# Optimization experiments

Measured on AMD Instinct MI355X. Metric: run time of the kernel, lower is better.

Reference implementation:

```python
import jax, jax.numpy as jnp
import numpy as np

# Sizes (must match setup_inputs)
N = 1024      # total residues (2 structures x 512)
B = 2         # num_structid
RPS = 512     # residues per sample
P = 32        # n_protein_patches
E_AB = B * P * P
E_ab = 131072 # downsampled residue-residue edges
DIM = 256
PDIM = 128
NB = 15       # distance RBF basis count
EPS = 1e-6


def _fourier(x, f):
    # GaussianFourierEncoding1D: x [..., 1], f [m] -> [..., 2m]
    ang = 2.0 * jnp.pi * x * f
    return jnp.concatenate([jnp.sin(ang), jnp.cos(ang)], axis=-1)


def _gelu_mlp(x, w1, b1, w2, b2):
    return jnp.dot(jax.nn.gelu(jnp.dot(x, w1) + b1), w2) + b2


def _frames(coords):
    # get_frame_matrix from N, CA, C atoms via Gram-Schmidt; coords [N,3,3]
    a, b, c = coords[:, 0], coords[:, 1], coords[:, 2]
    v1 = c - b
    v2 = a - b
    e1 = v1 / (jnp.linalg.norm(v1, axis=-1, keepdims=True) + EPS)
    u2 = v2 - e1 * jnp.sum(e1 * v2, axis=-1, keepdims=True)
    e2 = u2 / (jnp.linalg.norm(u2, axis=-1, keepdims=True) + EPS)
    e3 = jnp.cross(e1, e2)
    R = jnp.stack([e1, e2, e3], axis=-1)  # columns are the frame axes
    return R, b


def setup_inputs() -> dict:
    key = jax.random.key(0)
    ks = jax.random.split(key, 16)

    def lin(k, i, o):
        return (jax.random.normal(k, (i, o), jnp.float32) / np.sqrt(i)).astype(jnp.float32)

    # per-sample index offsets so gathers stay within each structure
    off_ab = (jnp.arange(E_ab) // (E_ab // B)).astype(jnp.int32) * RPS
    gather_idx_ab_a = jax.random.randint(ks[0], (E_ab,), 0, RPS, jnp.int32) + off_ab
    gather_idx_ab_b = jax.random.randint(ks[1], (E_ab,), 0, RPS, jnp.int32) + off_ab
    off_pid = (jnp.arange(B * P) // P).astype(jnp.int32) * RPS
    gather_idx_pid_a = jax.random.randint(ks[2], (B * P,), 0, RPS, jnp.int32) + off_pid

    return {
        "res_embedding_in": jax.random.normal(ks[3], (N, DIM), jnp.float32),
        "timestep_encoding_prot": jax.random.uniform(ks[4], (N, 1), jnp.float32),
        "input_protein_coords": jax.random.normal(ks[5], (N, 3, 3), jnp.float32) * 3.0,
        "time_freq": jax.random.normal(ks[6], (16,), jnp.float32),
        "chain_freq": jax.random.normal(ks[7], (PDIM // 4,), jnp.float32),
        "w1_res": lin(ks[8], DIM + 32, DIM),
        "b1_res": jnp.zeros((DIM,), jnp.float32),
        "w2_res": lin(ks[9], DIM, DIM),
        "b2_res": jnp.zeros((DIM,), jnp.float32),
        "w_geom": lin(ks[10], NB + 9 + 3, PDIM),
        "w1_edge": lin(ks[11], PDIM + PDIM // 2 + 2 * DIM, DIM),
        "b1_edge": jnp.zeros((DIM,), jnp.float32),
        "w2_edge": lin(ks[12], DIM, PDIM),
        "b2_edge": jnp.zeros((PDIM,), jnp.float32),
        "residue_index": (jnp.arange(N, dtype=jnp.int32) % 256),
        "res_chain_id": (jnp.arange(N, dtype=jnp.int32) // 256),
        "gather_idx_ab_a": gather_idx_ab_a,
        "gather_idx_ab_b": gather_idx_ab_b,
        "gather_idx_pid_a": gather_idx_pid_a,
    }


def reference(res_embedding_in, timestep_encoding_prot, input_protein_coords,
              time_freq, chain_freq,
              w1_res, b1_res, w2_res, b2_res,
              w_geom,
              w1_edge, b1_edge, w2_edge, b2_edge,
              residue_index, res_chain_id,
              gather_idx_ab_a, gather_idx_ab_b, gather_idx_pid_a):
    # residue representation: res_in_mlp(cat(emb, time_enc)) + emb
    te = _fourier(timestep_encoding_prot, time_freq)  # [N, 32]
    rep = _gelu_mlp(jnp.concatenate([res_embedding_in, te], axis=-1),
                    w1_res, b1_res, w2_res, b2_res) + res_embedding_in

    # patch-grid (AB) edge expansion, then merged edge list (ab first, AB second)
    pid = gather_idx_pid_a.reshape(B, P)
    AB_a = jnp.broadcast_to(pid[:, :, None], (B, P, P)).reshape(-1)
    AB_b = jnp.broadcast_to(pid[:, None, :], (B, P, P)).reshape(-1)
    src = jnp.concatenate([gather_idx_ab_a, AB_a])
    dst = jnp.concatenate([gather_idx_ab_b, AB_b])

    # chain relative positional encoding (_compute_chain_pe)
    ri = residue_index.astype(jnp.float32)
    disp = (ri[src] - ri[dst]) / 8.0                        # [E]
    rope = _fourier(disp[:, None], chain_freq) / (jnp.abs(disp) + 1.0)[:, None]
    rope = rope * (res_chain_id[src] == res_chain_id[dst])[:, None]  # [E, PDIM//2]

    # relative geometry encoding from backbone frames
    R, t = _frames(input_protein_coords)
    d = t[dst] - t[src]                                     # [E, 3]
    dist = jnp.sqrt(jnp.sum(d * d, axis=-1) + EPS)
    local = jnp.einsum('eik,ei->ek', R[src], d) / (dist + 1.0)[:, None]
    relrot = jnp.einsum('eia,eib->eab', R[src], R[dst]).reshape(-1, 9)
    centers = jnp.linspace(0.0, 20.0, NB)
    sig = 20.0 / NB
    rbf = jnp.exp(-0.5 * ((dist[:, None] - centers) / sig) ** 2)
    geom = jnp.dot(jnp.concatenate([rbf, relrot, local], axis=-1), w_geom)  # [E, PDIM]

    # pp_edge_embed(cat(geom, chain_pe, rep[src], rep[dst]))
    edge_in = jnp.concatenate([geom, rope, rep[src], rep[dst]], axis=-1)
    edge_reps = _gelu_mlp(edge_in, w1_edge, b1_edge, w2_edge, b2_edge)  # [E, PDIM]
    return edge_reps
```

## Files before the change

kernel.cpp:

```cpp
#include <hip/hip_runtime.h>


typedef __attribute__((ext_vector_type(8))) short short8;
typedef __attribute__((ext_vector_type(4))) float f32x4;

#define TWO_PI 6.283185307179586f
#define E_AB_TOT 131072

#define WS_RT    0
#define WS_REPB  49152
#define WS_W1F   573440
#define WS_W2F   884736
#define WS_PS    950272
#define WS_PD    1998848
#define WS_WG1   3047424

__device__ __forceinline__ unsigned short f2bf(float x){
  unsigned int u = __float_as_uint(x);
  u += 0x7fffu + ((u >> 16) & 1u);
  return (unsigned short)(u >> 16);
}

__device__ __forceinline__ unsigned int pack_bf16(float lo, float hi){
  unsigned int ul = __float_as_uint(lo), uh = __float_as_uint(hi);
  ul += 0x7fffu + ((ul >> 16) & 1u);
  uh += 0x7fffu + ((uh >> 16) & 1u);
  return __builtin_amdgcn_perm(uh, ul, 0x07060302);
}

__device__ __forceinline__ float gelu_s(float x){
  float s = x * x;
  float w = x * __builtin_fmaf(-0.1029437f, s, -2.30220847f);
  float e = __builtin_exp2f(w);
  return x * __builtin_amdgcn_rcpf(1.0f + e);
}

__global__ __launch_bounds__(256) void prep_k(
    const float* __restrict__ emb, const float* __restrict__ ts,
    const float* __restrict__ tf,  const float* __restrict__ w1,
    const float* __restrict__ b1,  const float* __restrict__ w2,
    const float* __restrict__ b2,  unsigned short* __restrict__ repb,
    const float* __restrict__ coords, float* __restrict__ RT,
    const float* __restrict__ wg, const float* __restrict__ w1e,
    unsigned short* __restrict__ w1f,
    const float* __restrict__ w2e, unsigned short* __restrict__ w2f,
    float* __restrict__ wg1){
  __shared__ float xt[288 * 12];
  __shared__ float ht[256 * 12];
  int blk = blockIdx.x, tid = threadIdx.x;
  if (blk < 128){
    int n0 = blk * 8;
    #pragma unroll
    for (int nd = 0; nd < 8; ++nd)
      xt[tid * 12 + nd] = emb[(n0 + nd) * 256 + tid];
    {
      int nd = tid >> 5, j = tid & 31;
      float ang = TWO_PI * ts[n0 + nd] * tf[j & 15];
      float s, c; __sincosf(ang, &s, &c);
      xt[(256 + j) * 12 + nd] = (j < 16) ? s : c;
    }
    __syncthreads();
    float acc[8];
    float bias1 = b1[tid];
    #pragma unroll
    for (int nd = 0; nd < 8; ++nd) acc[nd] = bias1;
    #pragma unroll 4
    for (int k = 0; k < 288; ++k){
      float w = w1[k * 256 + tid];
      f32x4 xa = *(const f32x4*)&xt[k * 12];
      f32x4 xb = *(const f32x4*)&xt[k * 12 + 4];
      acc[0] += xa[0]*w; acc[1] += xa[1]*w; acc[2] += xa[2]*w; acc[3] += xa[3]*w;
      acc[4] += xb[0]*w; acc[5] += xb[1]*w; acc[6] += xb[2]*w; acc[7] += xb[3]*w;
    }
    #pragma unroll
    for (int nd = 0; nd < 8; ++nd) ht[tid * 12 + nd] = gelu_s(acc[nd]);
    __syncthreads();
    float acc2[8];
    float bias2 = b2[tid];
    #pragma unroll
    for (int nd = 0; nd < 8; ++nd) acc2[nd] = bias2;
    #pragma unroll 4
    for (int k = 0; k < 256; ++k){
      float w = w2[k * 256 + tid];
      f32x4 ha = *(const f32x4*)&ht[k * 12];
      f32x4 hb = *(const f32x4*)&ht[k * 12 + 4];
      acc2[0] += ha[0]*w; acc2[1] += ha[1]*w; acc2[2] += ha[2]*w; acc2[3] += ha[3]*w;
      acc2[4] += hb[0]*w; acc2[5] += hb[1]*w; acc2[6] += hb[2]*w; acc2[7] += hb[3]*w;
    }
    #pragma unroll
    for (int nd = 0; nd < 8; ++nd)
      repb[(n0 + nd) * 256 + tid] = f2bf(acc2[nd] + xt[tid * 12 + nd]);
  } else if (blk < 132){
    int n = (blk - 128) * 256 + tid;
    const float* p = coords + n * 9;
    float ax=p[0],ay=p[1],az=p[2], bx=p[3],by=p[4],bz=p[5], cx=p[6],cy=p[7],cz=p[8];
    float v1x=cx-bx, v1y=cy-by, v1z=cz-bz;
    float v2x=ax-bx, v2y=ay-by, v2z=az-bz;
    float n1 = sqrtf(v1x*v1x+v1y*v1y+v1z*v1z) + 1e-6f;
    float e1x=v1x/n1, e1y=v1y/n1, e1z=v1z/n1;
    float dp = e1x*v2x + e1y*v2y + e1z*v2z;
    float u2x=v2x-e1x*dp, u2y=v2y-e1y*dp, u2z=v2z-e1z*dp;
    float n2 = sqrtf(u2x*u2x+u2y*u2y+u2z*u2z) + 1e-6f;
    float e2x=u2x/n2, e2y=u2y/n2, e2z=u2z/n2;
    float* r = RT + n * 12;
    r[0]=e1x; r[1]=e2x; r[2]=e1y*e2z - e1z*e2y;
    r[3]=e1y; r[4]=e2y; r[5]=e1z*e2x - e1x*e2z;
    r[6]=e1z; r[7]=e2z; r[8]=e1x*e2y - e1y*e2x;
    r[9]=bx;  r[10]=by; r[11]=bz;
  } else if (blk < 148){
    int u = (blk - 132) * 4 + (tid >> 6);
    int lane = tid & 63;
    int s = u >> 3, c = u & 7;
    int n  = c * 16 + (lane & 15);
    int kb = s * 32 + (lane >> 4) * 8;
    unsigned short* o = w2f + (((s * 8 + c) * 64) + lane) * 8;
    unsigned short vals[8];
    #pragma unroll
    for (int j = 0; j < 8; ++j)
      vals[j] = f2bf(w2e[(kb + j) * 128 + n]);
    *(uint4*)o = *(const uint4*)vals;
  } else if (blk < 220){
    int u = 16 + (blk - 148) * 4 + (tid >> 6);
    int lane = tid & 63;
    int s = u >> 4, c = u & 15;
    int n  = c * 16 + (lane & 15);
    int kb = s * 32 + (lane >> 4) * 8;
    unsigned short* o = w1f + (((s * 16 + c) * 64) + lane) * 8;
    unsigned short vals[8];
    for (int j = 0; j < 8; ++j){
      int k = kb + j;
      float val;
      if (k < 91)       val = w1e[(128 + k - 27)  * 256 + n];
      else if (k < 96)  val = 0.f;
      else if (k < 352) val = w1e[(192 + k - 96)  * 256 + n];
      else              val = w1e[(448 + k - 352) * 256 + n];
      vals[j] = f2bf(val);
    }
    *(uint4*)o = *(const uint4*)vals;
  } else {
    int b2_ = blk - 220;
    int n0 = b2_ * 16;
    float* slab = xt;
    #pragma unroll
    for (int i = 0; i < 8; ++i){
      int idx = tid + 256 * i;
      slab[idx] = w1e[(idx >> 4) * 256 + n0 + (idx & 15)];
    }
    __syncthreads();
    #pragma unroll
    for (int i = 0; i < 2; ++i){
      int o = tid + 256 * i;
      if (o < 432){
        int k = o >> 4, c = o & 15;
        float acc = 0.f;
        for (int j2 = 0; j2 < 128; ++j2)
          acc += wg[k * 128 + j2] * slab[j2 * 16 + c];
        wg1[k * 256 + n0 + c] = acc;
      }
    }
  }
}

__global__ __launch_bounds__(512) void proj_k(
    const unsigned short* __restrict__ repb,
    unsigned short* __restrict__ w1f,
    const float* __restrict__ b1e, const float* __restrict__ wg1,
    const float* __restrict__ w1e,
    float* __restrict__ ps, float* __restrict__ pd)
{
  if (blockIdx.x >= 32){
    int u = (blockIdx.x - 32) * 8 + (threadIdx.x >> 6);
    int lane = threadIdx.x & 63;
    int n  = u * 16 + (lane & 15);
    int kb = (lane >> 4) * 8;
    unsigned short* o = w1f + ((u * 64) + lane) * 8;
    unsigned short vals[8];
    #pragma unroll
    for (int j = 0; j < 8; ++j){
      int k = kb + j;
      float val = (k < 27) ? wg1[k * 256 + n] : w1e[(128 + k - 27) * 256 + n];
      vals[j] = f2bf(val);
    }
    *(uint4*)o = *(const uint4*)vals;
    return;
  }
  int part = blockIdx.x & 1;
  int nt   = blockIdx.x >> 1;
  int tid  = threadIdx.x, w = tid >> 6, lane = tid & 63;
  int c0 = w * 2, lr = lane & 15, quad = lane >> 4;
  int n0g = nt * 64;
  const short8* w1f8 = (const short8*)w1f;
  f32x4 acc[8];
  #pragma unroll
  for (int i = 0; i < 8; ++i) acc[i] = (f32x4){0.f, 0.f, 0.f, 0.f};
  int sb = 3 + part * 8;
  #pragma unroll
  for (int s = 0; s < 8; ++s){
    short8 a0 = w1f8[((sb + s) * 16 + c0 + 0) * 64 + lane];
    short8 a1 = w1f8[((sb + s) * 16 + c0 + 1) * 64 + lane];
    #pragma unroll
    for (int t = 0; t < 4; ++t){
      short8 b = *(const short8*)(repb + (n0g + t * 16 + lr) * 256 + s * 32 + quad * 8);
      acc[t]     = __builtin_amdgcn_mfma_f32_16x16x32_bf16(a0, b, acc[t],     0, 0, 0);
      acc[4 + t] = __builtin_amdgcn_mfma_f32_16x16x32_bf16(a1, b, acc[4 + t], 0, 0, 0);
    }
  }
  float* out = part ? pd : ps;
  #pragma unroll
  for (int c = 0; c < 2; ++c){
    f32x4 add = (f32x4){0.f, 0.f, 0.f, 0.f};
    if (!part) add = *(const f32x4*)(b1e + (c0 + c) * 16 + quad * 4);
    #pragma unroll
    for (int t = 0; t < 4; ++t){
      f32x4 v = acc[c * 4 + t];
      v[0] += add[0]; v[1] += add[1]; v[2] += add[2]; v[3] += add[3];
      *(f32x4*)(out + (n0g + t * 16 + lr) * 256 + w * 32 + quad * 8 + c * 4) = v;
    }
  }
}

__global__ __launch_bounds__(512, 8) void edge_k(
    const float* __restrict__ RT,  const float* __restrict__ cf,
    const int* __restrict__ resi, const int* __restrict__ chain,
    const int* __restrict__ gia,  const int* __restrict__ gib,
    const int* __restrict__ pid,
    const unsigned short* __restrict__ w1f, const unsigned short* __restrict__ w2f,
    const float* __restrict__ ps, const float* __restrict__ pd,
    const float* __restrict__ bias2,
    float* __restrict__ outp)
{
  __shared__ __align__(16) char smem[32768];
  __shared__ __align__(16) float rtbuf[128][12];
  __shared__ float scD[64];
  __shared__ float scI[64];
  __shared__ int lsrc[64];
  __shared__ int ldst[64];

  int tid = threadIdx.x;
  int e0  = blockIdx.x * 64;

  if (tid < 64){
    int e = e0 + tid, s_, d_;
    if (e < E_AB_TOT){ s_ = gia[e]; d_ = gib[e]; }
    else {
      int i = e - E_AB_TOT;
      int b = i >> 10, w_ = i & 1023;
      s_ = pid[b * 32 + (w_ >> 5)];
      d_ = pid[b * 32 + (w_ & 31)];
    }
    lsrc[tid] = s_; ldst[tid] = d_;
    float disp = ((float)resi[s_] - (float)resi[d_]) * 0.125f;
    scD[tid] = disp;
    scI[tid] = (chain[s_] == chain[d_]) ? 1.f / (fabsf(disp) + 1.f) : 0.f;
  } else if (tid < 192){
    int r  = tid - 64;
    int e  = e0 + (r & 63);
    int node;
    if (e < E_AB_TOT){ node = (r < 64) ? gia[e] : gib[e]; }
    else {
      int i = e - E_AB_TOT;
      int b = i >> 10, w_ = i & 1023;
      node = (r < 64) ? pid[b * 32 + (w_ >> 5)] : pid[b * 32 + (w_ & 31)];
    }
    const f32x4* p = (const f32x4*)(RT + node * 12);
    f32x4* q = (f32x4*)(&rtbuf[r][0]);
    q[0] = p[0]; q[1] = p[1]; q[2] = p[2];
  }
  __syncthreads();

  {
    #pragma unroll
    for (int it = 0; it < 4; ++it){
      int v = it * 512 + tid, ed = v >> 5, j = v & 31;
      float ang = TWO_PI * scD[ed] * cf[j];
      float s, c; __sincosf(ang, &s, &c);
      float inv = scI[ed];
      unsigned short* row = (unsigned short*)(smem + ed * 208);
      row[27 + j] = f2bf(s * inv);
      row[59 + j] = f2bf(c * inv);
    }
    #pragma unroll
    for (int it = 0; it < 2; ++it){
      int v = it * 512 + tid, ed = v >> 4, c = v & 15;
      float tx = rtbuf[64 + ed][9]  - rtbuf[ed][9];
      float ty = rtbuf[64 + ed][10] - rtbuf[ed][10];
      float tz = rtbuf[64 + ed][11] - rtbuf[ed][11];
      float dist = sqrtf(tx*tx + ty*ty + tz*tz + 1e-6f);
      if (c < 15){
        float z = (dist - (float)c * (20.f / 14.f)) * (15.f / 20.f);
        ((unsigned short*)(smem + ed * 208))[c] = f2bf(__expf(-0.5f * z * z));
      }
    }
    #pragma unroll
    for (int it = 0; it < 2; ++it){
      int v = it * 512 + tid, ed = v >> 4, cc = v & 15;
      if (cc < 12){
        const float* Rs = &rtbuf[ed][0];
        const float* Rd = &rtbuf[64 + ed][0];
        float val;
        if (cc < 9){
          int a  = (cc >= 6) ? 2 : ((cc >= 3) ? 1 : 0);
          int b_ = cc - 3 * a;
          val = Rs[a]*Rd[b_] + Rs[3+a]*Rd[3+b_] + Rs[6+a]*Rd[6+b_];
        } else {
          int k = cc - 9;
          float tx = Rd[9]-Rs[9], ty = Rd[10]-Rs[10], tz = Rd[11]-Rs[11];
          float dist = sqrtf(tx*tx + ty*ty + tz*tz + 1e-6f);
          val = (Rs[k]*tx + Rs[3+k]*ty + Rs[6+k]*tz) / (dist + 1.f);
        }
        ((unsigned short*)(smem + ed * 208))[15 + cc] = f2bf(val);
      }
    }
    {
      int ed = tid >> 3, c8 = tid & 7;
      ((unsigned short*)(smem + ed * 208))[91 + c8] = 0;
    }
  }
  __syncthreads();

  int w    = tid >> 6, lane = tid & 63;
  int c0   = w * 2;
  int lr   = lane & 15;
  int quad = lane >> 4, qoff = quad * 16;
  f32x4 acc[8];
  #pragma unroll
  for (int i = 0; i < 8; ++i) acc[i] = (f32x4){0.f, 0.f, 0.f, 0.f};
  const short8* w1f8 = (const short8*)w1f;

  #pragma unroll
  for (int s = 0; s < 3; ++s){
    short8 a0 = w1f8[(s * 16 + c0 + 0) * 64 + lane];
    short8 a1 = w1f8[(s * 16 + c0 + 1) * 64 + lane];
    short8 be0 = *(const short8*)(smem + ( 0 + lr) * 208 + s * 64 + qoff);
    short8 be1 = *(const short8*)(smem + (16 + lr) * 208 + s * 64 + qoff);
    short8 be2 = *(const short8*)(smem + (32 + lr) * 208 + s * 64 + qoff);
    short8 be3 = *(const short8*)(smem + (48 + lr) * 208 + s * 64 + qoff);
    acc[0] = __builtin_amdgcn_mfma_f32_16x16x32_bf16(a0, be0, acc[0], 0, 0, 0);
    acc[1] = __builtin_amdgcn_mfma_f32_16x16x32_bf16(a0, be1, acc[1], 0, 0, 0);
    acc[2] = __builtin_amdgcn_mfma_f32_16x16x32_bf16(a0, be2, acc[2], 0, 0, 0);
    acc[3] = __builtin_amdgcn_mfma_f32_16x16x32_bf16(a0, be3, acc[3], 0, 0, 0);
    acc[4] = __builtin_amdgcn_mfma_f32_16x16x32_bf16(a1, be0, acc[4], 0, 0, 0);
    acc[5] = __builtin_amdgcn_mfma_f32_16x16x32_bf16(a1, be1, acc[5], 0, 0, 0);
    acc[6] = __builtin_amdgcn_mfma_f32_16x16x32_bf16(a1, be2, acc[6], 0, 0, 0);
    acc[7] = __builtin_amdgcn_mfma_f32_16x16x32_bf16(a1, be3, acc[7], 0, 0, 0);
  }

  int offS[4], offD[4];
  #pragma unroll
  for (int t = 0; t < 4; ++t){
    offS[t] = lsrc[t * 16 + lr] * 256 + w * 32 + quad * 8;
    offD[t] = ldst[t * 16 + lr] * 256 + w * 32 + quad * 8;
  }
  __syncthreads();

  {
    char* Hb = smem;
    #pragma unroll
    for (int c = 0; c < 2; ++c){
      f32x4 pv[4], qv[4];
      #pragma unroll
      for (int t = 0; t < 4; ++t){
        pv[t] = *(const f32x4*)(ps + offS[t] + c * 4);
        qv[t] = *(const f32x4*)(pd + offD[t] + c * 4);
      }
      int n = (c0 + c) * 16 + quad * 4;
      #pragma unroll
      for (int t = 0; t < 4; ++t){
        int e = t * 16 + lr;
        f32x4 s4 = acc[c * 4 + t];
        float v0 = gelu_s(s4[0] + pv[t][0] + qv[t][0]);
        float v1 = gelu_s(s4[1] + pv[t][1] + qv[t][1]);
        float v2 = gelu_s(s4[2] + pv[t][2] + qv[t][2]);
        float v3 = gelu_s(s4[3] + pv[t][3] + qv[t][3]);
        uint2 p; p.x = pack_bf16(v0, v1); p.y = pack_bf16(v2, v3);
        *(uint2*)(Hb + ((e * 512 + n * 2) ^ ((e & 7) << 4))) = p;
      }
    }
  }
  __syncthreads();

  int c2 = (w & 3) * 2;
  int eb = (w >> 2) * 32;
  int hx = (lr & 7) << 4;
  f32x4 acc2[4];
  #pragma unroll
  for (int i = 0; i < 4; ++i) acc2[i] = (f32x4){0.f, 0.f, 0.f, 0.f};
  const short8* w2f8 = (const short8*)w2f;
  #pragma unroll
  for (int s = 0; s < 8; ++s){
    short8 aa0 = w2f8[(s * 8 + c2 + 0) * 64 + lane];
    short8 aa1 = w2f8[(s * 8 + c2 + 1) * 64 + lane];
    short8 h0 = *(const short8*)(smem + (((eb +  0 + lr) * 512 + s * 64 + qoff) ^ hx));
    short8 h1 = *(const short8*)(smem + (((eb + 16 + lr) * 512 + s * 64 + qoff) ^ hx));
    acc2[0] = __builtin_amdgcn_mfma_f32_16x16x32_bf16(aa0, h0, acc2[0], 0, 0, 0);
    acc2[1] = __builtin_amdgcn_mfma_f32_16x16x32_bf16(aa0, h1, acc2[1], 0, 0, 0);
    acc2[2] = __builtin_amdgcn_mfma_f32_16x16x32_bf16(aa1, h0, acc2[2], 0, 0, 0);
    acc2[3] = __builtin_amdgcn_mfma_f32_16x16x32_bf16(aa1, h1, acc2[3], 0, 0, 0);
  }

  {
    int n0 = c2 * 16 + quad * 4;
    f32x4 bz0 = *(const f32x4*)(bias2 + n0);
    f32x4 bz1 = *(const f32x4*)(bias2 + n0 + 16);
    float* og = outp + (size_t)e0 * 128;
    #pragma unroll
    for (int t = 0; t < 2; ++t){
      int e = eb + t * 16 + lr;
      f32x4 v0, v1;
      v0[0] = acc2[t][0] + bz0[0]; v0[1] = acc2[t][1] + bz0[1];
      v0[2] = acc2[t][2] + bz0[2]; v0[3] = acc2[t][3] + bz0[3];
      v1[0] = acc2[2 + t][0] + bz1[0]; v1[1] = acc2[2 + t][1] + bz1[1];
      v1[2] = acc2[2 + t][2] + bz1[2]; v1[3] = acc2[2 + t][3] + bz1[3];
      *(f32x4*)(og + (size_t)e * 128 + n0)      = v0;
      *(f32x4*)(og + (size_t)e * 128 + n0 + 16) = v1;
    }
  }
}

extern "C" void kernel_launch(void* const* d_in, const int* in_sizes, int n_in,
                              void* d_out, int out_size, void* d_ws, size_t ws_size,
                              hipStream_t stream) {
  const float* emb    = (const float*)d_in[0];
  const float* ts     = (const float*)d_in[1];
  const float* coords = (const float*)d_in[2];
  const float* tf     = (const float*)d_in[3];
  const float* cf     = (const float*)d_in[4];
  const float* w1r    = (const float*)d_in[5];
  const float* b1r    = (const float*)d_in[6];
  const float* w2r    = (const float*)d_in[7];
  const float* b2r    = (const float*)d_in[8];
  const float* wg     = (const float*)d_in[9];
  const float* w1e    = (const float*)d_in[10];
  const float* b1e    = (const float*)d_in[11];
  const float* w2e    = (const float*)d_in[12];
  const float* b2e    = (const float*)d_in[13];
  const int* resi     = (const int*)d_in[14];
  const int* chain    = (const int*)d_in[15];
  const int* gia      = (const int*)d_in[16];
  const int* gib      = (const int*)d_in[17];
  const int* pid      = (const int*)d_in[18];

  char* ws = (char*)d_ws;
  float* RT            = (float*)(ws + WS_RT);
  unsigned short* REPB = (unsigned short*)(ws + WS_REPB);
  unsigned short* W1F  = (unsigned short*)(ws + WS_W1F);
  unsigned short* W2F  = (unsigned short*)(ws + WS_W2F);
  float* PS            = (float*)(ws + WS_PS);
  float* PD            = (float*)(ws + WS_PD);
  float* WG1           = (float*)(ws + WS_WG1);
  float* outp          = (float*)d_out;

  hipLaunchKernelGGL(prep_k, dim3(236), dim3(256), 0, stream,
                     emb, ts, tf, w1r, b1r, w2r, b2r, REPB,
                     coords, RT, wg, w1e, W1F, w2e, W2F, WG1);
  hipLaunchKernelGGL(proj_k, dim3(34), dim3(512), 0, stream,
                     REPB, W1F, b1e, WG1, w1e, PS, PD);
  hipLaunchKernelGGL(edge_k, dim3(2080), dim3(512), 0, stream,
                     RT, cf, resi, chain, gia, gib, pid, W1F, W2F, PS, PD,
                     b2e, outp);
}
```

Before: 222.6 us.

## Prefetch projected gathers before MFMA, fuse geom-weight packing into prep, nontemporal output stores

The edge kernel now issues its gathered ps/pd loads before the first MFMA loop, so their latency overlaps with matrix work rather than sitting after it. The geometry-weight fold and its bf16 packing move from proj_k into prep_k through shared memory, which removes the WG1 workspace round trip and two proj_k blocks. The occupancy hint on edge_k drops from 8 to 4 to leave room for the 32 extra prefetch registers per thread, and output stores become nontemporal. The risk is lower occupancy reducing latency hiding elsewhere in the kernel.

```diff
diff --git a/kernel.cpp b/kernel.cpp
--- a/kernel.cpp
+++ b/kernel.cpp
@@ -13,7 +13,6 @@
 #define WS_W2F   884736
 #define WS_PS    950272
 #define WS_PD    1998848
-#define WS_WG1   3047424
 
 __device__ __forceinline__ unsigned short f2bf(float x){
   unsigned int u = __float_as_uint(x);
@@ -43,8 +42,7 @@
     const float* __restrict__ coords, float* __restrict__ RT,
     const float* __restrict__ wg, const float* __restrict__ w1e,
     unsigned short* __restrict__ w1f,
-    const float* __restrict__ w2e, unsigned short* __restrict__ w2f,
-    float* __restrict__ wg1){
+    const float* __restrict__ w2e, unsigned short* __restrict__ w2f){
   __shared__ float xt[288 * 12];
   __shared__ float ht[256 * 12];
   int blk = blockIdx.x, tid = threadIdx.x;
@@ -138,9 +136,10 @@
     }
     *(uint4*)o = *(const uint4*)vals;
   } else {
-    int b2_ = blk - 220;
-    int n0 = b2_ * 16;
+    int c = blk - 220;
+    int n0 = c * 16;
     float* slab = xt;
+    float* res  = ht;
     #pragma unroll
     for (int i = 0; i < 8; ++i){
       int idx = tid + 256 * i;
@@ -151,39 +150,37 @@
     for (int i = 0; i < 2; ++i){
       int o = tid + 256 * i;
       if (o < 432){
-        int k = o >> 4, c = o & 15;
+        int k = o >> 4, cc = o & 15;
         float acc = 0.f;
         for (int j2 = 0; j2 < 128; ++j2)
-          acc += wg[k * 128 + j2] * slab[j2 * 16 + c];
-        wg1[k * 256 + n0 + c] = acc;
+          acc += wg[k * 128 + j2] * slab[j2 * 16 + cc];
+        res[o] = acc;
       }
+    }
+    __syncthreads();
+    if (tid < 64){
+      int lane = tid;
+      int nn = lane & 15;
+      int kb = (lane >> 4) * 8;
+      unsigned short vals[8];
+      #pragma unroll
+      for (int j = 0; j < 8; ++j){
+        int k = kb + j;
+        float val = (k < 27) ? res[k * 16 + nn]
+                             : w1e[(128 + k - 27) * 256 + n0 + nn];
+        vals[j] = f2bf(val);
+      }
+      *(uint4*)(w1f + ((c * 64) + lane) * 8) = *(const uint4*)vals;
     }
   }
 }
 
 __global__ __launch_bounds__(512) void proj_k(
     const unsigned short* __restrict__ repb,
-    unsigned short* __restrict__ w1f,
-    const float* __restrict__ b1e, const float* __restrict__ wg1,
-    const float* __restrict__ w1e,
+    const unsigned short* __restrict__ w1f,
+    const float* __restrict__ b1e,
     float* __restrict__ ps, float* __restrict__ pd)
 {
-  if (blockIdx.x >= 32){
-    int u = (blockIdx.x - 32) * 8 + (threadIdx.x >> 6);
-    int lane = threadIdx.x & 63;
-    int n  = u * 16 + (lane & 15);
-    int kb = (lane >> 4) * 8;
-    unsigned short* o = w1f + ((u * 64) + lane) * 8;
-    unsigned short vals[8];
-    #pragma unroll
-    for (int j = 0; j < 8; ++j){
-      int k = kb + j;
-      float val = (k < 27) ? wg1[k * 256 + n] : w1e[(128 + k - 27) * 256 + n];
-      vals[j] = f2bf(val);
-    }
-    *(uint4*)o = *(const uint4*)vals;
-    return;
-  }
   int part = blockIdx.x & 1;
   int nt   = blockIdx.x >> 1;
   int tid  = threadIdx.x, w = tid >> 6, lane = tid & 63;
@@ -219,7 +216,7 @@
   }
 }
 
-__global__ __launch_bounds__(512, 8) void edge_k(
+__global__ __launch_bounds__(512, 4) void edge_k(
     const float* __restrict__ RT,  const float* __restrict__ cf,
     const int* __restrict__ resi, const int* __restrict__ chain,
     const int* __restrict__ gia,  const int* __restrict__ gib,
@@ -267,6 +264,11 @@
     q[0] = p[0]; q[1] = p[1]; q[2] = p[2];
   }
   __syncthreads();
+
+  int w    = tid >> 6, lane = tid & 63;
+  int c0   = w * 2;
+  int lr   = lane & 15;
+  int quad = lane >> 4, qoff = quad * 16;
 
   {
     #pragma unroll
@@ -316,12 +318,21 @@
       ((unsigned short*)(smem + ed * 208))[91 + c8] = 0;
     }
   }
+
+  f32x4 pv0[4], pv1[4], qv0[4], qv1[4];
+  {
+    #pragma unroll
+    for (int t = 0; t < 4; ++t){
+      int oS = lsrc[t * 16 + lr] * 256 + w * 32 + quad * 8;
+      int oD = ldst[t * 16 + lr] * 256 + w * 32 + quad * 8;
+      pv0[t] = *(const f32x4*)(ps + oS);
+      pv1[t] = *(const f32x4*)(ps + oS + 4);
+      qv0[t] = *(const f32x4*)(pd + oD);
+      qv1[t] = *(const f32x4*)(pd + oD + 4);
+    }
+  }
   __syncthreads();
 
-  int w    = tid >> 6, lane = tid & 63;
-  int c0   = w * 2;
-  int lr   = lane & 15;
-  int quad = lane >> 4, qoff = quad * 16;
   f32x4 acc[8];
   #pragma unroll
   for (int i = 0; i < 8; ++i) acc[i] = (f32x4){0.f, 0.f, 0.f, 0.f};
@@ -344,37 +355,29 @@
     acc[6] = __builtin_amdgcn_mfma_f32_16x16x32_bf16(a1, be2, acc[6], 0, 0, 0);
     acc[7] = __builtin_amdgcn_mfma_f32_16x16x32_bf16(a1, be3, acc[7], 0, 0, 0);
   }
-
-  int offS[4], offD[4];
-  #pragma unroll
-  for (int t = 0; t < 4; ++t){
-    offS[t] = lsrc[t * 16 + lr] * 256 + w * 32 + quad * 8;
-    offD[t] = ldst[t * 16 + lr] * 256 + w * 32 + quad * 8;
-  }
   __syncthreads();
 
   {
     char* Hb = smem;
     #pragma unroll
-    for (int c = 0; c < 2; ++c){
-      f32x4 pv[4], qv[4];
-      #pragma unroll
-      for (int t = 0; t < 4; ++t){
-        pv[t] = *(const f32x4*)(ps + offS[t] + c * 4);
-        qv[t] = *(const f32x4*)(pd + offD[t] + c * 4);
-      }
-      int n = (c0 + c) * 16 + quad * 4;
-      #pragma unroll
-      for (int t = 0; t < 4; ++t){
-        int e = t * 16 + lr;
-        f32x4 s4 = acc[c * 4 + t];
-        float v0 = gelu_s(s4[0] + pv[t][0] + qv[t][0]);
-        float v1 = gelu_s(s4[1] + pv[t][1] + qv[t][1]);
-        float v2 = gelu_s(s4[2] + pv[t][2] + qv[t][2]);
-        float v3 = gelu_s(s4[3] + pv[t][3] + qv[t][3]);
-        uint2 p; p.x = pack_bf16(v0, v1); p.y = pack_bf16(v2, v3);
-        *(uint2*)(Hb + ((e * 512 + n * 2) ^ ((e & 7) << 4))) = p;
-      }
+    for (int t = 0; t < 4; ++t){
+      int e = t * 16 + lr;
+      int n0 = c0 * 16 + quad * 4;
+      f32x4 s0 = acc[t];
+      float a0 = gelu_s(s0[0] + pv0[t][0] + qv0[t][0]);
+      float a1 = gelu_s(s0[1] + pv0[t][1] + qv0[t][1]);
+      float a2 = gelu_s(s0[2] + pv0[t][2] + qv0[t][2]);
+      float a3 = gelu_s(s0[3] + pv0[t][3] + qv0[t][3]);
+      uint2 p0; p0.x = pack_bf16(a0, a1); p0.y = pack_bf16(a2, a3);
+      *(uint2*)(Hb + ((e * 512 + n0 * 2) ^ ((e & 7) << 4))) = p0;
+      int n1 = (c0 + 1) * 16 + quad * 4;
+      f32x4 s1 = acc[4 + t];
+      float b0 = gelu_s(s1[0] + pv1[t][0] + qv1[t][0]);
+      float b1 = gelu_s(s1[1] + pv1[t][1] + qv1[t][1]);
+      float b2 = gelu_s(s1[2] + pv1[t][2] + qv1[t][2]);
+      float b3 = gelu_s(s1[3] + pv1[t][3] + qv1[t][3]);
+      uint2 p1; p1.x = pack_bf16(b0, b1); p1.y = pack_bf16(b2, b3);
+      *(uint2*)(Hb + ((e * 512 + n1 * 2) ^ ((e & 7) << 4))) = p1;
     }
   }
   __syncthreads();
@@ -411,8 +414,8 @@
       v0[2] = acc2[t][2] + bz0[2]; v0[3] = acc2[t][3] + bz0[3];
       v1[0] = acc2[2 + t][0] + bz1[0]; v1[1] = acc2[2 + t][1] + bz1[1];
       v1[2] = acc2[2 + t][2] + bz1[2]; v1[3] = acc2[2 + t][3] + bz1[3];
-      *(f32x4*)(og + (size_t)e * 128 + n0)      = v0;
-      *(f32x4*)(og + (size_t)e * 128 + n0 + 16) = v1;
+      __builtin_nontemporal_store(v0, (f32x4*)(og + (size_t)e * 128 + n0));
+      __builtin_nontemporal_store(v1, (f32x4*)(og + (size_t)e * 128 + n0 + 16));
     }
   }
 }
@@ -447,14 +450,13 @@
   unsigned short* W2F  = (unsigned short*)(ws + WS_W2F);
   float* PS            = (float*)(ws + WS_PS);
   float* PD            = (float*)(ws + WS_PD);
-  float* WG1           = (float*)(ws + WS_WG1);
   float* outp          = (float*)d_out;
 
   hipLaunchKernelGGL(prep_k, dim3(236), dim3(256), 0, stream,
                      emb, ts, tf, w1r, b1r, w2r, b2r, REPB,
-                     coords, RT, wg, w1e, W1F, w2e, W2F, WG1);
-  hipLaunchKernelGGL(proj_k, dim3(34), dim3(512), 0, stream,
-                     REPB, W1F, b1e, WG1, w1e, PS, PD);
+                     coords, RT, wg, w1e, W1F, w2e, W2F);
+  hipLaunchKernelGGL(proj_k, dim3(32), dim3(512), 0, stream,
+                     REPB, W1F, b1e, PS, PD);
   hipLaunchKernelGGL(edge_k, dim3(2080), dim3(512), 0, stream,
                      RT, cf, resi, chain, gia, gib, pid, W1F, W2F, PS, PD,
                      b2e, outp);
```

Result: slower. 233.5 us (+4.9%).

## Fuse geometry-weight packing into prep, halve residue MLP rows per block

Applied to the files above, without the earlier changes.

The residue MLP in prep_k now handles 4 residues per block across 256 blocks instead of 8 across 128, giving more parallelism to the small dense stage. The fused geometry weight (w_geom times w1_edge slice) is now packed straight into the bf16 MFMA fragment layout inside prep_k, which removes the WG1 workspace round trip and the extra blocks in proj_k. The edge kernel's shared buffer grows and its launch-bounds occupancy hint drops from 8 to 4, which changes register allocation and may reduce resident waves.

```diff
diff --git a/kernel.cpp b/kernel.cpp
--- a/kernel.cpp
+++ b/kernel.cpp
@@ -13,7 +13,6 @@
 #define WS_W2F   884736
 #define WS_PS    950272
 #define WS_PD    1998848
-#define WS_WG1   3047424
 
 __device__ __forceinline__ unsigned short f2bf(float x){
   unsigned int u = __float_as_uint(x);
@@ -43,55 +42,50 @@
     const float* __restrict__ coords, float* __restrict__ RT,
     const float* __restrict__ wg, const float* __restrict__ w1e,
     unsigned short* __restrict__ w1f,
-    const float* __restrict__ w2e, unsigned short* __restrict__ w2f,
-    float* __restrict__ wg1){
+    const float* __restrict__ w2e, unsigned short* __restrict__ w2f){
   __shared__ float xt[288 * 12];
   __shared__ float ht[256 * 12];
   int blk = blockIdx.x, tid = threadIdx.x;
-  if (blk < 128){
-    int n0 = blk * 8;
-    #pragma unroll
-    for (int nd = 0; nd < 8; ++nd)
+  if (blk < 256){
+    int n0 = blk * 4;
+    #pragma unroll
+    for (int nd = 0; nd < 4; ++nd)
       xt[tid * 12 + nd] = emb[(n0 + nd) * 256 + tid];
-    {
+    if (tid < 128){
       int nd = tid >> 5, j = tid & 31;
       float ang = TWO_PI * ts[n0 + nd] * tf[j & 15];
       float s, c; __sincosf(ang, &s, &c);
       xt[(256 + j) * 12 + nd] = (j < 16) ? s : c;
     }
     __syncthreads();
-    float acc[8];
+    float acc[4];
     float bias1 = b1[tid];
     #pragma unroll
-    for (int nd = 0; nd < 8; ++nd) acc[nd] = bias1;
-    #pragma unroll 4
+    for (int nd = 0; nd < 4; ++nd) acc[nd] = bias1;
+    #pragma unroll 8
     for (int k = 0; k < 288; ++k){
       float w = w1[k * 256 + tid];
       f32x4 xa = *(const f32x4*)&xt[k * 12];
-      f32x4 xb = *(const f32x4*)&xt[k * 12 + 4];
       acc[0] += xa[0]*w; acc[1] += xa[1]*w; acc[2] += xa[2]*w; acc[3] += xa[3]*w;
-      acc[4] += xb[0]*w; acc[5] += xb[1]*w; acc[6] += xb[2]*w; acc[7] += xb[3]*w;
-    }
-    #pragma unroll
-    for (int nd = 0; nd < 8; ++nd) ht[tid * 12 + nd] = gelu_s(acc[nd]);
+    }
+    #pragma unroll
+    for (int nd = 0; nd < 4; ++nd) ht[tid * 12 + nd] = gelu_s(acc[nd]);
     __syncthreads();
-    float acc2[8];
+    float acc2[4];
     float bias2 = b2[tid];
     #pragma unroll
-    for (int nd = 0; nd < 8; ++nd) acc2[nd] = bias2;
-    #pragma unroll 4
+    for (int nd = 0; nd < 4; ++nd) acc2[nd] = bias2;
+    #pragma unroll 8
     for (int k = 0; k < 256; ++k){
       float w = w2[k * 256 + tid];
       f32x4 ha = *(const f32x4*)&ht[k * 12];
-      f32x4 hb = *(const f32x4*)&ht[k * 12 + 4];
       acc2[0] += ha[0]*w; acc2[1] += ha[1]*w; acc2[2] += ha[2]*w; acc2[3] += ha[3]*w;
-      acc2[4] += hb[0]*w; acc2[5] += hb[1]*w; acc2[6] += hb[2]*w; acc2[7] += hb[3]*w;
-    }
-    #pragma unroll
-    for (int nd = 0; nd < 8; ++nd)
+    }
+    #pragma unroll
+    for (int nd = 0; nd < 4; ++nd)
       repb[(n0 + nd) * 256 + tid] = f2bf(acc2[nd] + xt[tid * 12 + nd]);
-  } else if (blk < 132){
-    int n = (blk - 128) * 256 + tid;
+  } else if (blk < 260){
+    int n = (blk - 256) * 256 + tid;
     const float* p = coords + n * 9;
     float ax=p[0],ay=p[1],az=p[2], bx=p[3],by=p[4],bz=p[5], cx=p[6],cy=p[7],cz=p[8];
     float v1x=cx-bx, v1y=cy-by, v1z=cz-bz;
@@ -107,8 +101,8 @@
     r[3]=e1y; r[4]=e2y; r[5]=e1z*e2x - e1x*e2z;
     r[6]=e1z; r[7]=e2z; r[8]=e1x*e2y - e1y*e2x;
     r[9]=bx;  r[10]=by; r[11]=bz;
-  } else if (blk < 148){
-    int u = (blk - 132) * 4 + (tid >> 6);
+  } else if (blk < 276){
+    int u = (blk - 260) * 4 + (tid >> 6);
     int lane = tid & 63;
     int s = u >> 3, c = u & 7;
     int n  = c * 16 + (lane & 15);
@@ -119,8 +113,8 @@
     for (int j = 0; j < 8; ++j)
       vals[j] = f2bf(w2e[(kb + j) * 128 + n]);
     *(uint4*)o = *(const uint4*)vals;
-  } else if (blk < 220){
-    int u = 16 + (blk - 148) * 4 + (tid >> 6);
+  } else if (blk < 348){
+    int u = 16 + (blk - 276) * 4 + (tid >> 6);
     int lane = tid & 63;
     int s = u >> 4, c = u & 15;
     int n  = c * 16 + (lane & 15);
@@ -138,9 +132,10 @@
     }
     *(uint4*)o = *(const uint4*)vals;
   } else {
-    int b2_ = blk - 220;
-    int n0 = b2_ * 16;
+    int c = blk - 348;
+    int n0 = c * 16;
     float* slab = xt;
+    float* res  = ht;
     #pragma unroll
     for (int i = 0; i < 8; ++i){
       int idx = tid + 256 * i;
@@ -151,39 +146,37 @@
     for (int i = 0; i < 2; ++i){
       int o = tid + 256 * i;
       if (o < 432){
-        int k = o >> 4, c = o & 15;
+        int k = o >> 4, cc = o & 15;
         float acc = 0.f;
         for (int j2 = 0; j2 < 128; ++j2)
-          acc += wg[k * 128 + j2] * slab[j2 * 16 + c];
-        wg1[k * 256 + n0 + c] = acc;
-      }
+          acc += wg[k * 128 + j2] * slab[j2 * 16 + cc];
+        res[o] = acc;
+      }
+    }
+    __syncthreads();
+    if (tid < 64){
+      int lane = tid;
+      int nn = lane & 15;
+      int kb = (lane >> 4) * 8;
+      unsigned short vals[8];
+      #pragma unroll
+      for (int j = 0; j < 8; ++j){
+        int k = kb + j;
+        float val = (k < 27) ? res[k * 16 + nn]
+                             : w1e[(128 + k - 27) * 256 + n0 + nn];
+        vals[j] = f2bf(val);
+      }
+      *(uint4*)(w1f + ((c * 64) + lane) * 8) = *(const uint4*)vals;
     }
   }
 }
 
 __global__ __launch_bounds__(512) void proj_k(
     const unsigned short* __restrict__ repb,
-    unsigned short* __restrict__ w1f,
-    const float* __restrict__ b1e, const float* __restrict__ wg1,
-    const float* __restrict__ w1e,
+    const unsigned short* __restrict__ w1f,
+    const float* __restrict__ b1e,
     float* __restrict__ ps, float* __restrict__ pd)
 {
-  if (blockIdx.x >= 32){
-    int u = (blockIdx.x - 32) * 8 + (threadIdx.x >> 6);
-    int lane = threadIdx.x & 63;
-    int n  = u * 16 + (lane & 15);
-    int kb = (lane >> 4) * 8;
-    unsigned short* o = w1f + ((u * 64) + lane) * 8;
-    unsigned short vals[8];
-    #pragma unroll
-    for (int j = 0; j < 8; ++j){
-      int k = kb + j;
-      float val = (k < 27) ? wg1[k * 256 + n] : w1e[(128 + k - 27) * 256 + n];
-      vals[j] = f2bf(val);
-    }
-    *(uint4*)o = *(const uint4*)vals;
-    return;
-  }
   int part = blockIdx.x & 1;
   int nt   = blockIdx.x >> 1;
   int tid  = threadIdx.x, w = tid >> 6, lane = tid & 63;
@@ -219,7 +212,7 @@
   }
 }
 
-__global__ __launch_bounds__(512, 8) void edge_k(
+__global__ __launch_bounds__(512, 4) void edge_k(
     const float* __restrict__ RT,  const float* __restrict__ cf,
     const int* __restrict__ resi, const int* __restrict__ chain,
     const int* __restrict__ gia,  const int* __restrict__ gib,
@@ -229,7 +222,7 @@
     const float* __restrict__ bias2,
     float* __restrict__ outp)
 {
-  __shared__ __align__(16) char smem[32768];
+  __shared__ __align__(16) char smem[36864];
   __shared__ __align__(16) float rtbuf[128][12];
   __shared__ float scD[64];
   __shared__ float scI[64];
@@ -267,6 +260,11 @@
     q[0] = p[0]; q[1] = p[1]; q[2] = p[2];
   }
   __syncthreads();
+
+  int w    = tid >> 6, lane = tid & 63;
+  int c0   = w * 2;
+  int lr   = lane & 15;
+  int quad = lane >> 4, qoff = quad * 16;
 
   {
     #pragma unroll
@@ -318,10 +316,6 @@
   }
   __syncthreads();
 
-  int w    = tid >> 6, lane = tid & 63;
-  int c0   = w * 2;
-  int lr   = lane & 15;
-  int quad = lane >> 4, qoff = quad * 16;
   f32x4 acc[8];
   #pragma unroll
   for (int i = 0; i < 8; ++i) acc[i] = (f32x4){0.f, 0.f, 0.f, 0.f};
@@ -447,14 +441,13 @@
   unsigned short* W2F  = (unsigned short*)(ws + WS_W2F);
   float* PS            = (float*)(ws + WS_PS);
   float* PD            = (float*)(ws + WS_PD);
-  float* WG1           = (float*)(ws + WS_WG1);
   float* outp          = (float*)d_out;
 
-  hipLaunchKernelGGL(prep_k, dim3(236), dim3(256), 0, stream,
+  hipLaunchKernelGGL(prep_k, dim3(364), dim3(256), 0, stream,
                      emb, ts, tf, w1r, b1r, w2r, b2r, REPB,
-                     coords, RT, wg, w1e, W1F, w2e, W2F, WG1);
-  hipLaunchKernelGGL(proj_k, dim3(34), dim3(512), 0, stream,
-                     REPB, W1F, b1e, WG1, w1e, PS, PD);
+                     coords, RT, wg, w1e, W1F, w2e, W2F);
+  hipLaunchKernelGGL(proj_k, dim3(32), dim3(512), 0, stream,
+                     REPB, W1F, b1e, PS, PD);
   hipLaunchKernelGGL(edge_k, dim3(2080), dim3(512), 0, stream,
                      RT, cf, resi, chain, gia, gib, pid, W1F, W2F, PS, PD,
                      b2e, outp);
```

After: 202.8 us. -8.9%, faster.
